# Kernel tuning notes

Measured on AMD Instinct MI355X. Metric: run time of the kernel, lower is better.

## Reference

```python
import jax, jax.numpy as jnp
import numpy as np

B, T, D = 4, 4096, 512

def setup_inputs() -> dict:
    key = jax.random.key(0)
    k1, k2, k3 = jax.random.split(key, 3)
    z_hat = jax.random.normal(k1, (B, T, D), dtype=jnp.float32)
    P = jax.random.uniform(k2, (B, T), dtype=jnp.float32)
    lengths = jax.random.randint(k3, (B,), 0, T).astype(jnp.int32)
    return {"z_hat": z_hat, "P": P, "lengths": lengths}

def reference(z_hat, P, lengths):
    # z_hat: [B, T, D], P: [B, T], lengths: [B]
    Bs, Tc, _ = z_hat.shape
    P_clamped = jnp.clip(P, 0.0, 1.0 - 1e-6)
    q = 1.0 - P_clamped
    # inclusive cumulative sum of log q (same as padded-cumsum[:,1:] in torch)
    log_cumprod_q = jnp.cumsum(jnp.log(q), axis=1)                 # [B, T]
    log_P = jnp.log(jnp.clip(P_clamped, 1e-6, None))               # [B, T]
    # log_M[b, t, k] = log P[b, k] + logcum[b, t] - logcum[b, k], causal (k <= t)
    log_M = (log_P[:, None, :]
             + log_cumprod_q[:, :, None]
             - log_cumprod_q[:, None, :])                          # [B, T, T]
    t_idx = jnp.arange(Tc)
    causal = t_idx[:, None] >= t_idx[None, :]                      # k <= t kept
    M = jnp.where(causal[None, :, :], jnp.exp(log_M), 0.0)         # [B, T, T]
    z_bar = jnp.einsum('btk,bkd->btd', M, z_hat)                   # [B, T, D]
    padding_mask = t_idx[None, :] < lengths[:, None]               # [B, T]
    return z_bar * padding_mask[:, :, None].astype(z_bar.dtype)
```

## Files before the change

### kernel.cpp

```cpp
#include <hip/hip_runtime.h>


#define CHUNK 16
#define NCMAX 512

__global__ __launch_bounds__(128) void k_local(
    const float* __restrict__ z, const float* __restrict__ P,
    const int* __restrict__ lengths,
    float* __restrict__ S, float* __restrict__ A,
    float* __restrict__ out, int B, int T, int D4, int NC) {
  const int blk = blockIdx.x;
  const int b = blk / NC, c = blk % NC;
  const int t0 = c * CHUNK;
  const int tid = threadIdx.x;
  const int L = lengths[b];
  const int nt = min(CHUNK, T - t0);
  const float4 zero = make_float4(0.f, 0.f, 0.f, 0.f);
  const size_t rowbase = ((size_t)b * T + t0) * D4;

  if (t0 >= L) {
    float4* o4 = (float4*)out;
    if (tid < D4)
      for (int t = 0; t < nt; ++t) o4[rowbase + (size_t)t * D4 + tid] = zero;
    return;
  }

  __shared__ float p_s[CHUNK], q_s[CHUNK];
  if (tid < CHUNK) {
    int tg = t0 + tid;
    float p = (tg < T) ? P[(size_t)b * T + tg] : 0.0f;
    p = fminf(fmaxf(p, 0.0f), 1.0f - 1e-6f);
    q_s[tid] = 1.0f - p;
    p_s[tid] = fmaxf(p, 1e-6f);
  }
  __syncthreads();

  if (tid < D4) {
    const float4* z4 = (const float4*)z;
    float4 zr[CHUNK];
#pragma unroll
    for (int t = 0; t < CHUNK; ++t)
      if (t < nt) zr[t] = z4[rowbase + (size_t)t * D4 + tid];
    float4 s = zero;
#pragma unroll
    for (int t = 0; t < CHUNK; ++t)
      if (t < nt) {
        float q = q_s[t], pe = p_s[t];
        s.x = fmaf(q, s.x, pe * zr[t].x);
        s.y = fmaf(q, s.y, pe * zr[t].y);
        s.z = fmaf(q, s.z, pe * zr[t].z);
        s.w = fmaf(q, s.w, pe * zr[t].w);
      }
    ((float4*)S)[((size_t)b * NC + c) * D4 + tid] = s;
  }
  if (tid == 0) {
    float r = 1.0f;
    for (int t = 0; t < nt; ++t) r *= q_s[t];
    A[b * NC + c] = r;
  }
}

__global__ __launch_bounds__(128) void k_apply(
    const float* __restrict__ z, const float* __restrict__ P,
    const float* __restrict__ S, const float* __restrict__ A,
    const int* __restrict__ lengths, float* __restrict__ out,
    int B, int T, int D4, int NC) {
  const int blk = blockIdx.x;
  const int b = blk / NC, c = blk % NC;
  const int t0 = c * CHUNK;
  const int tid = threadIdx.x;
  const int L = lengths[b];
  if (t0 >= L) return;
  const int nt = min(CHUNK, T - t0);
  const float4 zero = make_float4(0.f, 0.f, 0.f, 0.f);

  __shared__ float p_s[CHUNK], q_s[CHUNK];
  __shared__ float a_s[256];
  __shared__ float w_s[256];

  if (tid < CHUNK) {
    int tg = t0 + tid;
    float p = (tg < T) ? P[(size_t)b * T + tg] : 0.0f;
    p = fminf(fmaxf(p, 0.0f), 1.0f - 1e-6f);
    q_s[tid] = 1.0f - p;
    p_s[tid] = fmaxf(p, 1e-6f);
  }
  for (int i = tid; i < NC; i += 128) a_s[i] = A[b * NC + i];
  __syncthreads();

  {
    int i0 = tid, i1 = tid + 128;
    w_s[i0] = (i0 < c - 1) ? a_s[i0 + 1] : 1.0f;
    w_s[i1] = (i1 < c - 1) ? a_s[i1 + 1] : 1.0f;
    __syncthreads();
#pragma unroll
    for (int off = 1; off < 256; off <<= 1) {
      float v0 = (i0 + off < 256) ? w_s[i0 + off] : 1.0f;
      float v1 = (i1 + off < 256) ? w_s[i1 + off] : 1.0f;
      __syncthreads();
      w_s[i0] *= v0;
      w_s[i1] *= v1;
      __syncthreads();
    }
  }

  if (tid < D4) {
    const float4* S4 = (const float4*)S + (size_t)b * NC * D4 + tid;
    float4 a0 = zero, a1 = zero, a2 = zero, a3 = zero;
    int cp = 0;
    for (; cp + 4 <= c; cp += 4) {
      float w0 = w_s[cp], w1 = w_s[cp + 1], w2 = w_s[cp + 2], w3 = w_s[cp + 3];
      float4 r0 = S4[(size_t)cp * D4];
      float4 r1 = S4[(size_t)(cp + 1) * D4];
      float4 r2 = S4[(size_t)(cp + 2) * D4];
      float4 r3 = S4[(size_t)(cp + 3) * D4];
      a0.x = fmaf(w0, r0.x, a0.x); a0.y = fmaf(w0, r0.y, a0.y);
      a0.z = fmaf(w0, r0.z, a0.z); a0.w = fmaf(w0, r0.w, a0.w);
      a1.x = fmaf(w1, r1.x, a1.x); a1.y = fmaf(w1, r1.y, a1.y);
      a1.z = fmaf(w1, r1.z, a1.z); a1.w = fmaf(w1, r1.w, a1.w);
      a2.x = fmaf(w2, r2.x, a2.x); a2.y = fmaf(w2, r2.y, a2.y);
      a2.z = fmaf(w2, r2.z, a2.z); a2.w = fmaf(w2, r2.w, a2.w);
      a3.x = fmaf(w3, r3.x, a3.x); a3.y = fmaf(w3, r3.y, a3.y);
      a3.z = fmaf(w3, r3.z, a3.z); a3.w = fmaf(w3, r3.w, a3.w);
    }
    for (; cp < c; ++cp) {
      float w = w_s[cp];
      float4 r = S4[(size_t)cp * D4];
      a0.x = fmaf(w, r.x, a0.x); a0.y = fmaf(w, r.y, a0.y);
      a0.z = fmaf(w, r.z, a0.z); a0.w = fmaf(w, r.w, a0.w);
    }
    float4 s;
    s.x = (a0.x + a1.x) + (a2.x + a3.x);
    s.y = (a0.y + a1.y) + (a2.y + a3.y);
    s.z = (a0.z + a1.z) + (a2.z + a3.z);
    s.w = (a0.w + a1.w) + (a2.w + a3.w);

    const size_t rowbase = ((size_t)b * T + t0) * D4;
    const float4* z4 = (const float4*)z;
    float4* o4 = (float4*)out;
#pragma unroll
    for (int t = 0; t < CHUNK; ++t)
      if (t < nt) {
        float4 zv = z4[rowbase + (size_t)t * D4 + tid];
        float q = q_s[t], pe = p_s[t];
        s.x = fmaf(q, s.x, pe * zv.x);
        s.y = fmaf(q, s.y, pe * zv.y);
        s.z = fmaf(q, s.z, pe * zv.z);
        s.w = fmaf(q, s.w, pe * zv.w);
        float4 o = ((t0 + t) < L) ? s : zero;
        o4[rowbase + (size_t)t * D4 + tid] = o;
      }
  }
}


__global__ __launch_bounds__(128) void f_local(
    const float* __restrict__ z, const float* __restrict__ P,
    const int* __restrict__ lengths,
    float* __restrict__ S, float* __restrict__ A,
    int B, int T, int D, int NC) {
  int blk = blockIdx.x;
  int b = blk / NC, c = blk % NC;
  int t0 = c * CHUNK;
  int tid = threadIdx.x;
  int D4 = D >> 2;
  float4* S4 = (float4*)(S + ((size_t)b * NC + c) * D);
  int L = lengths[b];
  if (t0 >= L) {
    float4 zero = make_float4(0.f, 0.f, 0.f, 0.f);
    for (int d4 = tid; d4 < D4; d4 += blockDim.x) S4[d4] = zero;
    if (tid == 0) A[b * NC + c] = 1.0f;
    return;
  }
  __shared__ float p_s[CHUNK], q_s[CHUNK];
  if (tid < CHUNK) {
    int tg = t0 + tid;
    float p = (tg < T) ? P[(size_t)b * T + tg] : 0.0f;
    p = fminf(fmaxf(p, 0.0f), 1.0f - 1e-6f);
    q_s[tid] = 1.0f - p;
    p_s[tid] = fmaxf(p, 1e-6f);
  }
  __syncthreads();
  int nt = min(CHUNK, T - t0);
  const float4* z4 = (const float4*)(z + ((size_t)b * T + t0) * D);
  for (int d4 = tid; d4 < D4; d4 += blockDim.x) {
    float4 s = make_float4(0.f, 0.f, 0.f, 0.f);
#pragma unroll
    for (int t = 0; t < CHUNK; ++t) {
      if (t < nt) {
        float4 zv = z4[(size_t)t * D4 + d4];
        float q = q_s[t], pe = p_s[t];
        s.x = fmaf(q, s.x, pe * zv.x);
        s.y = fmaf(q, s.y, pe * zv.y);
        s.z = fmaf(q, s.z, pe * zv.z);
        s.w = fmaf(q, s.w, pe * zv.w);
      }
    }
    S4[d4] = s;
  }
  if (tid == 0) {
    float r = 1.0f;
    for (int t = 0; t < nt; ++t) r *= q_s[t];
    A[b * NC + c] = r;
  }
}

__global__ void f_carry(
    const float* __restrict__ S, const float* __restrict__ A,
    float* __restrict__ Carry, int D4, int NC) {
  int b = blockIdx.x / D4;
  int d4 = blockIdx.x % D4;
  int c = threadIdx.x;
  __shared__ float sh_a[NCMAX];
  __shared__ float4 sh_v[NCMAX];
  float a = A[b * NC + c];
  const float4* S4 = (const float4*)S;
  float4 sv = S4[((size_t)b * NC + c) * D4 + d4];
  sh_a[c] = a;
  sh_v[c] = sv;
  __syncthreads();
  for (int off = 1; off < NC; off <<= 1) {
    float ap = 1.0f;
    float4 vp = make_float4(0.f, 0.f, 0.f, 0.f);
    bool has = (c >= off);
    if (has) { ap = sh_a[c - off]; vp = sh_v[c - off]; }
    __syncthreads();
    if (has) {
      sv.x = fmaf(a, vp.x, sv.x);
      sv.y = fmaf(a, vp.y, sv.y);
      sv.z = fmaf(a, vp.z, sv.z);
      sv.w = fmaf(a, vp.w, sv.w);
      a *= ap;
      sh_a[c] = a;
      sh_v[c] = sv;
    }
    __syncthreads();
  }
  float4 car = make_float4(0.f, 0.f, 0.f, 0.f);
  if (c > 0) car = sh_v[c - 1];
  float4* C4 = (float4*)Carry;
  C4[((size_t)b * NC + c) * D4 + d4] = car;
}

__global__ __launch_bounds__(128) void f_apply(
    const float* __restrict__ z, const float* __restrict__ P,
    const float* __restrict__ Carry, const int* __restrict__ lengths,
    float* __restrict__ out,
    int B, int T, int D, int NC) {
  int blk = blockIdx.x;
  int b = blk / NC, c = blk % NC;
  int t0 = c * CHUNK;
  int tid = threadIdx.x;
  int D4 = D >> 2;
  int nt = min(CHUNK, T - t0);
  float4* o4 = (float4*)(out + ((size_t)b * T + t0) * D);
  int L = lengths[b];
  if (t0 >= L) {
    float4 zero = make_float4(0.f, 0.f, 0.f, 0.f);
    for (int t = 0; t < nt; ++t)
      for (int d4 = tid; d4 < D4; d4 += blockDim.x)
        o4[(size_t)t * D4 + d4] = zero;
    return;
  }
  __shared__ float p_s[CHUNK], q_s[CHUNK];
  if (tid < CHUNK) {
    int tg = t0 + tid;
    float p = (tg < T) ? P[(size_t)b * T + tg] : 0.0f;
    p = fminf(fmaxf(p, 0.0f), 1.0f - 1e-6f);
    q_s[tid] = 1.0f - p;
    p_s[tid] = fmaxf(p, 1e-6f);
  }
  __syncthreads();
  const float4* z4 = (const float4*)(z + ((size_t)b * T + t0) * D);
  const float4* C4 = (const float4*)(Carry + ((size_t)b * NC + c) * D);
  for (int d4 = tid; d4 < D4; d4 += blockDim.x) {
    float4 s = C4[d4];
#pragma unroll
    for (int t = 0; t < CHUNK; ++t) {
      if (t < nt) {
        float4 zv = z4[(size_t)t * D4 + d4];
        float q = q_s[t], pe = p_s[t];
        s.x = fmaf(q, s.x, pe * zv.x);
        s.y = fmaf(q, s.y, pe * zv.y);
        s.z = fmaf(q, s.z, pe * zv.z);
        s.w = fmaf(q, s.w, pe * zv.w);
        float4 o = ((t0 + t) < L) ? s : make_float4(0.f, 0.f, 0.f, 0.f);
        o4[(size_t)t * D4 + d4] = o;
      }
    }
  }
}

extern "C" void kernel_launch(void* const* d_in, const int* in_sizes, int n_in,
                              void* d_out, int out_size, void* d_ws, size_t ws_size,
                              hipStream_t stream) {
  const float* z = (const float*)d_in[0];
  const float* P = (const float*)d_in[1];
  const int* lengths = (const int*)d_in[2];
  float* out = (float*)d_out;

  int B = in_sizes[2];
  int T = in_sizes[1] / B;
  int D = in_sizes[0] / in_sizes[1];
  int NC = (T + CHUNK - 1) / CHUNK;
  int D4 = D >> 2;

  float* S = (float*)d_ws;
  float* A = S + (size_t)B * NC * D;
  float* Carry = A + (((size_t)B * NC + 3) & ~(size_t)3);

  if ((D & 3) == 0 && D4 >= 1 && D4 <= 128 && NC >= 1 && NC <= 256) {
    dim3 grid(B * NC), block(128);
    k_local<<<grid, block, 0, stream>>>(z, P, lengths, S, A, out, B, T, D4, NC);
    k_apply<<<grid, block, 0, stream>>>(z, P, S, A, lengths, out, B, T, D4, NC);
    return;
  }

  f_local<<<dim3(B * NC), dim3(128), 0, stream>>>(z, P, lengths, S, A, B, T, D, NC);
  f_carry<<<dim3(B * D4), dim3(NC), 0, stream>>>(S, A, Carry, D4, NC);
  f_apply<<<dim3(B * NC), dim3(128), 0, stream>>>(z, P, Carry, lengths, out, B, T, D, NC);
}
```

Baseline: 105.2 us.

## Replace two-pass chunked scan with single-pass decoupled look-back scan kernel

Adds a single kernel that computes each chunk's local aggregate, publishes it with a flag, then looks back over predecessor chunks (up to four at a time via wave shuffles) to get an inclusive prefix, and writes the output in the same pass. This drops the second read of z and the per-block recomputation of weights over all previous chunk aggregates that the two-kernel path needed. It also uses nontemporal loads and stores and stops publishing once the chunk passes the sequence length. The cost is spin-waiting on atomics, which assumes earlier blocks are scheduled first and make progress, plus an extra memset launch to clear the flags.

```diff
diff --git a/kernel.cpp b/kernel.cpp
--- a/kernel.cpp
+++ b/kernel.cpp
@@ -2,7 +2,161 @@
 
 
 #define CHUNK 16
-#define NCMAX 512
+
+typedef float f4 __attribute__((ext_vector_type(4)));
+
+__global__ __launch_bounds__(128, 2) void k_scan(
+    const float* __restrict__ z, const float* __restrict__ P,
+    const int* __restrict__ lengths,
+    int* __restrict__ state, float* __restrict__ Apub,
+    float* __restrict__ Sagg, float* __restrict__ Pfx,
+    float* __restrict__ out, int B, int T, int NC) {
+  const int blk = blockIdx.x;
+  const int b = blk / NC, c = blk % NC;
+  const int t0 = c * CHUNK;
+  const int tid = threadIdx.x;
+  const int L = lengths[b];
+  const int nt = min(CHUNK, T - t0);
+  const f4 zero = {0.f, 0.f, 0.f, 0.f};
+  f4* o4 = (f4*)out;
+  const size_t rowbase = ((size_t)b * T + t0) * 128;
+
+  if (t0 >= L) {
+    for (int t = 0; t < nt; ++t)
+      __builtin_nontemporal_store(zero, &o4[rowbase + (size_t)t * 128 + tid]);
+    return;
+  }
+
+  const int nlive = min(nt, L - t0);
+
+  __shared__ float p_s[CHUNK], q_s[CHUNK];
+  if (tid < CHUNK) {
+    float p = (tid < nlive) ? P[(size_t)b * T + t0 + tid] : 0.0f;
+    p = fminf(fmaxf(p, 0.0f), 1.0f - 1e-6f);
+    q_s[tid] = 1.0f - p;
+    p_s[tid] = fmaxf(p, 1e-6f);
+  }
+  __syncthreads();
+
+  const f4* z4 = (const f4*)z;
+  f4 zr[CHUNK];
+#pragma unroll
+  for (int t = 0; t < CHUNK; ++t)
+    if (t < nlive)
+      zr[t] = __builtin_nontemporal_load(&z4[rowbase + (size_t)t * 128 + tid]);
+  f4 s = zero;
+  float a = 1.0f;
+#pragma unroll
+  for (int t = 0; t < CHUNK; ++t)
+    if (t < nlive) {
+      float q = q_s[t], pe = p_s[t];
+      s.x = fmaf(q, s.x, pe * zr[t].x);
+      s.y = fmaf(q, s.y, pe * zr[t].y);
+      s.z = fmaf(q, s.z, pe * zr[t].z);
+      s.w = fmaf(q, s.w, pe * zr[t].w);
+      a *= q;
+    }
+
+  const int idx = b * NC + c;
+  const bool next_live = (t0 + CHUNK < L) && (c + 1 < NC);
+  f4* Sg4 = (f4*)Sagg;
+  f4* Pf4 = (f4*)Pfx;
+
+  if (c > 0 && next_live) {
+    Sg4[(size_t)idx * 128 + tid] = s;
+    if (tid == 0) Apub[idx] = a;
+    __syncthreads();
+    if (tid == 0) {
+      __threadfence();
+      __hip_atomic_store(&state[idx], 1, __ATOMIC_RELEASE, __HIP_MEMORY_SCOPE_AGENT);
+    }
+  }
+
+  f4 carry = zero;
+  if (c > 0) {
+    const int base = b * NC;
+    const int lane = tid & 63;
+    const f4* Sg4c = (const f4*)Sagg;
+    const f4* Pf4c = (const f4*)Pfx;
+    float W = 1.0f;
+    int cp = c - 1;
+    for (;;) {
+      int nb = (cp >= 3) ? 4 : (cp + 1);
+      int off = (lane < nb) ? lane : 0;
+      int stv = __hip_atomic_load(&state[base + cp - off], __ATOMIC_ACQUIRE,
+                                  __HIP_MEMORY_SCOPE_AGENT);
+      int s0 = __shfl(stv, 0);
+      if (s0 == 0) continue;
+      int st1 = (nb > 1) ? __shfl(stv, 1) : 0;
+      int st2 = (nb > 2) ? __shfl(stv, 2) : 0;
+      int st3 = (nb > 3) ? __shfl(stv, 3) : 0;
+      int k = 1;
+      if (st1 != 0) { k = 2; if (st2 != 0) { k = 3; if (st3 != 0) k = 4; } }
+      int m = -1;
+      if (s0 == 2) m = 0;
+      else if (k > 1 && st1 == 2) m = 1;
+      else if (k > 2 && st2 == 2) m = 2;
+      else if (k > 3 && st3 == 2) m = 3;
+      int stop = (m >= 0) ? m : (k - 1);
+      float av = Apub[base + cp - off];
+      float aa[4];
+      aa[0] = __shfl(av, 0); aa[1] = __shfl(av, 1);
+      aa[2] = __shfl(av, 2); aa[3] = __shfl(av, 3);
+      f4 rr[4];
+#pragma unroll
+      for (int i = 0; i < 4; ++i) {
+        int ii = (i <= stop) ? i : stop;
+        size_t ro = (size_t)(base + cp - ii) * 128 + tid;
+        rr[i] = (ii == m) ? Pf4c[ro] : Sg4c[ro];
+      }
+      bool fin = false;
+#pragma unroll
+      for (int i = 0; i < 4; ++i) {
+        if (i <= stop && !fin) {
+          carry.x = fmaf(W, rr[i].x, carry.x);
+          carry.y = fmaf(W, rr[i].y, carry.y);
+          carry.z = fmaf(W, rr[i].z, carry.z);
+          carry.w = fmaf(W, rr[i].w, carry.w);
+          if (i == m) fin = true;
+          else W *= aa[i];
+        }
+      }
+      if (fin) break;
+      cp -= k;
+      if (cp < 0) break;
+    }
+  }
+
+  if (next_live) {
+    f4 f;
+    f.x = fmaf(a, carry.x, s.x);
+    f.y = fmaf(a, carry.y, s.y);
+    f.z = fmaf(a, carry.z, s.z);
+    f.w = fmaf(a, carry.w, s.w);
+    Pf4[(size_t)idx * 128 + tid] = f;
+    __syncthreads();
+    if (tid == 0) {
+      __threadfence();
+      __hip_atomic_store(&state[idx], 2, __ATOMIC_RELEASE, __HIP_MEMORY_SCOPE_AGENT);
+    }
+  }
+
+  f4 sc = carry;
+#pragma unroll
+  for (int t = 0; t < CHUNK; ++t) {
+    if (t < nlive) {
+      float q = q_s[t], pe = p_s[t];
+      sc.x = fmaf(q, sc.x, pe * zr[t].x);
+      sc.y = fmaf(q, sc.y, pe * zr[t].y);
+      sc.z = fmaf(q, sc.z, pe * zr[t].z);
+      sc.w = fmaf(q, sc.w, pe * zr[t].w);
+      __builtin_nontemporal_store(sc, &o4[rowbase + (size_t)t * 128 + tid]);
+    } else if (t < nt) {
+      __builtin_nontemporal_store(zero, &o4[rowbase + (size_t)t * 128 + tid]);
+    }
+  }
+}
+
 
 __global__ __launch_bounds__(128) void k_local(
     const float* __restrict__ z, const float* __restrict__ P,
@@ -24,7 +178,6 @@
       for (int t = 0; t < nt; ++t) o4[rowbase + (size_t)t * D4 + tid] = zero;
     return;
   }
-
   __shared__ float p_s[CHUNK], q_s[CHUNK];
   if (tid < CHUNK) {
     int tg = t0 + tid;
@@ -34,22 +187,18 @@
     p_s[tid] = fmaxf(p, 1e-6f);
   }
   __syncthreads();
-
   if (tid < D4) {
     const float4* z4 = (const float4*)z;
-    float4 zr[CHUNK];
-#pragma unroll
-    for (int t = 0; t < CHUNK; ++t)
-      if (t < nt) zr[t] = z4[rowbase + (size_t)t * D4 + tid];
     float4 s = zero;
 #pragma unroll
     for (int t = 0; t < CHUNK; ++t)
       if (t < nt) {
+        float4 zv = z4[rowbase + (size_t)t * D4 + tid];
         float q = q_s[t], pe = p_s[t];
-        s.x = fmaf(q, s.x, pe * zr[t].x);
-        s.y = fmaf(q, s.y, pe * zr[t].y);
-        s.z = fmaf(q, s.z, pe * zr[t].z);
-        s.w = fmaf(q, s.w, pe * zr[t].w);
+        s.x = fmaf(q, s.x, pe * zv.x);
+        s.y = fmaf(q, s.y, pe * zv.y);
+        s.z = fmaf(q, s.z, pe * zv.z);
+        s.w = fmaf(q, s.w, pe * zv.w);
       }
     ((float4*)S)[((size_t)b * NC + c) * D4 + tid] = s;
   }
@@ -85,9 +234,8 @@
     q_s[tid] = 1.0f - p;
     p_s[tid] = fmaxf(p, 1e-6f);
   }
-  for (int i = tid; i < NC; i += 128) a_s[i] = A[b * NC + i];
+  for (int i = tid; i < NC && i < 256; i += 128) a_s[i] = A[b * NC + i];
   __syncthreads();
-
   {
     int i0 = tid, i1 = tid + 128;
     w_s[i0] = (i0 < c - 1) ? a_s[i0 + 1] : 1.0f;
@@ -103,7 +251,6 @@
       __syncthreads();
     }
   }
-
   if (tid < D4) {
     const float4* S4 = (const float4*)S + (size_t)b * NC * D4 + tid;
     float4 a0 = zero, a1 = zero, a2 = zero, a3 = zero;
@@ -134,7 +281,6 @@
     s.y = (a0.y + a1.y) + (a2.y + a3.y);
     s.z = (a0.z + a1.z) + (a2.z + a3.z);
     s.w = (a0.w + a1.w) + (a2.w + a3.w);
-
     const size_t rowbase = ((size_t)b * T + t0) * D4;
     const float4* z4 = (const float4*)z;
     float4* o4 = (float4*)out;
@@ -153,144 +299,6 @@
   }
 }
 
-
-__global__ __launch_bounds__(128) void f_local(
-    const float* __restrict__ z, const float* __restrict__ P,
-    const int* __restrict__ lengths,
-    float* __restrict__ S, float* __restrict__ A,
-    int B, int T, int D, int NC) {
-  int blk = blockIdx.x;
-  int b = blk / NC, c = blk % NC;
-  int t0 = c * CHUNK;
-  int tid = threadIdx.x;
-  int D4 = D >> 2;
-  float4* S4 = (float4*)(S + ((size_t)b * NC + c) * D);
-  int L = lengths[b];
-  if (t0 >= L) {
-    float4 zero = make_float4(0.f, 0.f, 0.f, 0.f);
-    for (int d4 = tid; d4 < D4; d4 += blockDim.x) S4[d4] = zero;
-    if (tid == 0) A[b * NC + c] = 1.0f;
-    return;
-  }
-  __shared__ float p_s[CHUNK], q_s[CHUNK];
-  if (tid < CHUNK) {
-    int tg = t0 + tid;
-    float p = (tg < T) ? P[(size_t)b * T + tg] : 0.0f;
-    p = fminf(fmaxf(p, 0.0f), 1.0f - 1e-6f);
-    q_s[tid] = 1.0f - p;
-    p_s[tid] = fmaxf(p, 1e-6f);
-  }
-  __syncthreads();
-  int nt = min(CHUNK, T - t0);
-  const float4* z4 = (const float4*)(z + ((size_t)b * T + t0) * D);
-  for (int d4 = tid; d4 < D4; d4 += blockDim.x) {
-    float4 s = make_float4(0.f, 0.f, 0.f, 0.f);
-#pragma unroll
-    for (int t = 0; t < CHUNK; ++t) {
-      if (t < nt) {
-        float4 zv = z4[(size_t)t * D4 + d4];
-        float q = q_s[t], pe = p_s[t];
-        s.x = fmaf(q, s.x, pe * zv.x);
-        s.y = fmaf(q, s.y, pe * zv.y);
-        s.z = fmaf(q, s.z, pe * zv.z);
-        s.w = fmaf(q, s.w, pe * zv.w);
-      }
-    }
-    S4[d4] = s;
-  }
-  if (tid == 0) {
-    float r = 1.0f;
-    for (int t = 0; t < nt; ++t) r *= q_s[t];
-    A[b * NC + c] = r;
-  }
-}
-
-__global__ void f_carry(
-    const float* __restrict__ S, const float* __restrict__ A,
-    float* __restrict__ Carry, int D4, int NC) {
-  int b = blockIdx.x / D4;
-  int d4 = blockIdx.x % D4;
-  int c = threadIdx.x;
-  __shared__ float sh_a[NCMAX];
-  __shared__ float4 sh_v[NCMAX];
-  float a = A[b * NC + c];
-  const float4* S4 = (const float4*)S;
-  float4 sv = S4[((size_t)b * NC + c) * D4 + d4];
-  sh_a[c] = a;
-  sh_v[c] = sv;
-  __syncthreads();
-  for (int off = 1; off < NC; off <<= 1) {
-    float ap = 1.0f;
-    float4 vp = make_float4(0.f, 0.f, 0.f, 0.f);
-    bool has = (c >= off);
-    if (has) { ap = sh_a[c - off]; vp = sh_v[c - off]; }
-    __syncthreads();
-    if (has) {
-      sv.x = fmaf(a, vp.x, sv.x);
-      sv.y = fmaf(a, vp.y, sv.y);
-      sv.z = fmaf(a, vp.z, sv.z);
-      sv.w = fmaf(a, vp.w, sv.w);
-      a *= ap;
-      sh_a[c] = a;
-      sh_v[c] = sv;
-    }
-    __syncthreads();
-  }
-  float4 car = make_float4(0.f, 0.f, 0.f, 0.f);
-  if (c > 0) car = sh_v[c - 1];
-  float4* C4 = (float4*)Carry;
-  C4[((size_t)b * NC + c) * D4 + d4] = car;
-}
-
-__global__ __launch_bounds__(128) void f_apply(
-    const float* __restrict__ z, const float* __restrict__ P,
-    const float* __restrict__ Carry, const int* __restrict__ lengths,
-    float* __restrict__ out,
-    int B, int T, int D, int NC) {
-  int blk = blockIdx.x;
-  int b = blk / NC, c = blk % NC;
-  int t0 = c * CHUNK;
-  int tid = threadIdx.x;
-  int D4 = D >> 2;
-  int nt = min(CHUNK, T - t0);
-  float4* o4 = (float4*)(out + ((size_t)b * T + t0) * D);
-  int L = lengths[b];
-  if (t0 >= L) {
-    float4 zero = make_float4(0.f, 0.f, 0.f, 0.f);
-    for (int t = 0; t < nt; ++t)
-      for (int d4 = tid; d4 < D4; d4 += blockDim.x)
-        o4[(size_t)t * D4 + d4] = zero;
-    return;
-  }
-  __shared__ float p_s[CHUNK], q_s[CHUNK];
-  if (tid < CHUNK) {
-    int tg = t0 + tid;
-    float p = (tg < T) ? P[(size_t)b * T + tg] : 0.0f;
-    p = fminf(fmaxf(p, 0.0f), 1.0f - 1e-6f);
-    q_s[tid] = 1.0f - p;
-    p_s[tid] = fmaxf(p, 1e-6f);
-  }
-  __syncthreads();
-  const float4* z4 = (const float4*)(z + ((size_t)b * T + t0) * D);
-  const float4* C4 = (const float4*)(Carry + ((size_t)b * NC + c) * D);
-  for (int d4 = tid; d4 < D4; d4 += blockDim.x) {
-    float4 s = C4[d4];
-#pragma unroll
-    for (int t = 0; t < CHUNK; ++t) {
-      if (t < nt) {
-        float4 zv = z4[(size_t)t * D4 + d4];
-        float q = q_s[t], pe = p_s[t];
-        s.x = fmaf(q, s.x, pe * zv.x);
-        s.y = fmaf(q, s.y, pe * zv.y);
-        s.z = fmaf(q, s.z, pe * zv.z);
-        s.w = fmaf(q, s.w, pe * zv.w);
-        float4 o = ((t0 + t) < L) ? s : make_float4(0.f, 0.f, 0.f, 0.f);
-        o4[(size_t)t * D4 + d4] = o;
-      }
-    }
-  }
-}
-
 extern "C" void kernel_launch(void* const* d_in, const int* in_sizes, int n_in,
                               void* d_out, int out_size, void* d_ws, size_t ws_size,
                               hipStream_t stream) {
@@ -304,19 +312,25 @@
   int D = in_sizes[0] / in_sizes[1];
   int NC = (T + CHUNK - 1) / CHUNK;
   int D4 = D >> 2;
+  size_t nidx = (size_t)B * NC;
+  size_t nidx4 = (nidx + 3) & ~(size_t)3;
+
+  int* state = (int*)d_ws;
+  float* Apub = (float*)d_ws + nidx4;
+  float* Sagg = Apub + nidx4;
+  float* Pfx = Sagg + nidx * D;
+  size_t need = (nidx4 * 2 + nidx * (size_t)D * 2) * sizeof(float);
+
+  if (D4 == 128 && nidx >= 1 && nidx <= 2048 && ws_size >= need) {
+    (void)hipMemsetAsync(state, 0, nidx * sizeof(int), stream);
+    k_scan<<<dim3((int)nidx), dim3(128), 0, stream>>>(
+        z, P, lengths, state, Apub, Sagg, Pfx, out, B, T, NC);
+    return;
+  }
 
   float* S = (float*)d_ws;
-  float* A = S + (size_t)B * NC * D;
-  float* Carry = A + (((size_t)B * NC + 3) & ~(size_t)3);
-
-  if ((D & 3) == 0 && D4 >= 1 && D4 <= 128 && NC >= 1 && NC <= 256) {
-    dim3 grid(B * NC), block(128);
-    k_local<<<grid, block, 0, stream>>>(z, P, lengths, S, A, out, B, T, D4, NC);
-    k_apply<<<grid, block, 0, stream>>>(z, P, S, A, lengths, out, B, T, D4, NC);
-    return;
-  }
-
-  f_local<<<dim3(B * NC), dim3(128), 0, stream>>>(z, P, lengths, S, A, B, T, D, NC);
-  f_carry<<<dim3(B * D4), dim3(NC), 0, stream>>>(S, A, Carry, D4, NC);
-  f_apply<<<dim3(B * NC), dim3(128), 0, stream>>>(z, P, Carry, lengths, out, B, T, D, NC);
+  float* A = S + nidx * D;
+  dim3 grid((int)nidx), block(128);
+  k_local<<<grid, block, 0, stream>>>(z, P, lengths, S, A, out, B, T, D4, NC);
+  k_apply<<<grid, block, 0, stream>>>(z, P, S, A, lengths, out, B, T, D4, NC);
 }
```

Measured after the change: 250.0 us. 2.38x slower.

## Use 64-row chunks with 4 row-groups per block and warp-shuffle carry scan

Applied to the files above, without the earlier changes.

Replaces the 16-row chunked scan with 64-row chunks handled by 512-thread blocks split into four 16-row groups that combine partial states through shared memory. Fewer chunks shrink the per-batch carry buffer and let the chunk-weight prefix product run as a single 64-lane shuffle scan instead of a barrier-heavy shared-memory scan. The apply kernel prefetches z rows before the carry sum, splits that sum across groups, and writes output with nontemporal stores. The cost is more registers per thread, fewer blocks in the grid, and the local pass now skips S/A for chunks the apply pass does not need.

```diff
diff --git a/kernel.cpp b/kernel.cpp
--- a/kernel.cpp
+++ b/kernel.cpp
@@ -1,20 +1,215 @@
 #include <hip/hip_runtime.h>
 
 
-#define CHUNK 16
-#define NCMAX 512
-
-__global__ __launch_bounds__(128) void k_local(
+#define CHUNK 64
+#define GR 16
+#define NG 4
+#define NCMAX 64
+
+#define FB_CHUNK 16
+#define FB_NCMAX 256
+
+typedef float f4 __attribute__((ext_vector_type(4)));
+
+__global__ __launch_bounds__(512) void kl64(
+    const float* __restrict__ z, const float* __restrict__ P,
+    const int* __restrict__ lengths,
+    float* __restrict__ S, float* __restrict__ A,
+    float* __restrict__ out, int B, int T, int NC) {
+  const int blk = blockIdx.x;
+  const int b = blk / NC, c = blk % NC;
+  const int t0 = c * CHUNK;
+  const int tid = threadIdx.x;
+  const int col = tid & 127, g = tid >> 7;
+  const int L = lengths[b];
+  const int nt = min(CHUNK, T - t0);
+  const f4 zero = {0.f, 0.f, 0.f, 0.f};
+  f4* o4 = (f4*)out;
+  const size_t rowbase = ((size_t)b * T + t0) * 128;
+
+  if (t0 >= L) {
+    for (int r = g; r < nt; r += NG)
+      __builtin_nontemporal_store(zero, &o4[rowbase + (size_t)r * 128 + col]);
+    return;
+  }
+
+  __shared__ float p_s[CHUNK], q_s[CHUNK];
+  __shared__ float ga_s[NG];
+  __shared__ f4 gs_s[NG][128];
+
+  if (tid < CHUNK) {
+    int tg = t0 + tid;
+    float p = (tg < T) ? P[(size_t)b * T + tg] : 0.0f;
+    p = fminf(fmaxf(p, 0.0f), 1.0f - 1e-6f);
+    q_s[tid] = 1.0f - p;
+    p_s[tid] = fmaxf(p, 1e-6f);
+  }
+  __syncthreads();
+
+  const int r0 = g * GR;
+  const int ng = min(GR, nt - r0);
+  const f4* z4 = (const f4*)z;
+  f4 zr[GR];
+#pragma unroll
+  for (int j = 0; j < GR; ++j)
+    if (j < ng) zr[j] = z4[rowbase + (size_t)(r0 + j) * 128 + col];
+  f4 s = zero;
+  float a = 1.0f;
+#pragma unroll
+  for (int j = 0; j < GR; ++j)
+    if (j < ng) {
+      float q = q_s[r0 + j], pe = p_s[r0 + j];
+      s.x = fmaf(q, s.x, pe * zr[j].x);
+      s.y = fmaf(q, s.y, pe * zr[j].y);
+      s.z = fmaf(q, s.z, pe * zr[j].z);
+      s.w = fmaf(q, s.w, pe * zr[j].w);
+      a *= q;
+    }
+  gs_s[g][col] = s;
+  if (col == 0) ga_s[g] = a;
+  __syncthreads();
+
+  if ((t0 + CHUNK < L) && (c + 1 < NC)) {
+    if (g == NG - 1) {
+      f4 x = gs_s[0][col];
+#pragma unroll
+      for (int j = 1; j < NG; ++j) {
+        float aj = ga_s[j];
+        f4 sj = gs_s[j][col];
+        x.x = fmaf(aj, x.x, sj.x);
+        x.y = fmaf(aj, x.y, sj.y);
+        x.z = fmaf(aj, x.z, sj.z);
+        x.w = fmaf(aj, x.w, sj.w);
+      }
+      ((f4*)S)[((size_t)b * NC + c) * 128 + col] = x;
+    }
+    if (tid == 0) A[b * NC + c] = ga_s[0] * ga_s[1] * ga_s[2] * ga_s[3];
+  }
+}
+
+__global__ __launch_bounds__(512) void ka64(
+    const float* __restrict__ z, const float* __restrict__ P,
+    const float* __restrict__ S, const float* __restrict__ A,
+    const int* __restrict__ lengths, float* __restrict__ out,
+    int B, int T, int NC) {
+  const int blk = blockIdx.x;
+  const int b = blk / NC, c = blk % NC;
+  const int t0 = c * CHUNK;
+  const int tid = threadIdx.x;
+  const int col = tid & 127, g = tid >> 7;
+  const int L = lengths[b];
+  if (t0 >= L) return;
+  const int nt = min(CHUNK, T - t0);
+  const f4 zero = {0.f, 0.f, 0.f, 0.f};
+
+  __shared__ float p_s[CHUNK], q_s[CHUNK];
+  __shared__ float sp_s[NCMAX + 1];
+  __shared__ float ga_s[NG];
+  __shared__ f4 gs_s[NG][128];
+  __shared__ f4 part_s[NG][128];
+
+  const int r0 = g * GR;
+  const int ng = min(GR, nt - r0);
+  const f4* z4 = (const f4*)z;
+  const size_t rowbase = ((size_t)b * T + t0) * 128;
+  f4 zr[GR];
+#pragma unroll
+  for (int j = 0; j < GR; ++j)
+    if (j < ng) zr[j] = z4[rowbase + (size_t)(r0 + j) * 128 + col];
+
+  if (tid < CHUNK) {
+    int tg = t0 + tid;
+    float p = (tg < T) ? P[(size_t)b * T + tg] : 0.0f;
+    p = fminf(fmaxf(p, 0.0f), 1.0f - 1e-6f);
+    q_s[tid] = 1.0f - p;
+    p_s[tid] = fmaxf(p, 1e-6f);
+  }
+  if (tid < 64) {
+    const int lane = tid;
+    float y = (lane < c) ? A[b * NC + lane] : 1.0f;
+#pragma unroll
+    for (int off = 1; off < 64; off <<= 1) {
+      float t = __shfl_down(y, off);
+      if (lane + off < 64) y *= t;
+    }
+    sp_s[lane] = y;
+  }
+  __syncthreads();
+
+  f4 acc = zero;
+  const f4* S4 = (const f4*)S;
+  for (int cp = g; cp < c; cp += NG) {
+    float w = sp_s[cp + 1];
+    f4 r = S4[((size_t)b * NC + cp) * 128 + col];
+    acc.x = fmaf(w, r.x, acc.x);
+    acc.y = fmaf(w, r.y, acc.y);
+    acc.z = fmaf(w, r.z, acc.z);
+    acc.w = fmaf(w, r.w, acc.w);
+  }
+  part_s[g][col] = acc;
+
+  f4 s = zero;
+  float a = 1.0f;
+#pragma unroll
+  for (int j = 0; j < GR; ++j)
+    if (j < ng) {
+      float q = q_s[r0 + j], pe = p_s[r0 + j];
+      s.x = fmaf(q, s.x, pe * zr[j].x);
+      s.y = fmaf(q, s.y, pe * zr[j].y);
+      s.z = fmaf(q, s.z, pe * zr[j].z);
+      s.w = fmaf(q, s.w, pe * zr[j].w);
+      a *= q;
+    }
+  gs_s[g][col] = s;
+  if (col == 0) ga_s[g] = a;
+  __syncthreads();
+
+  f4 carry = part_s[0][col];
+  {
+    f4 p1 = part_s[1][col], p2 = part_s[2][col], p3 = part_s[3][col];
+    carry.x = (carry.x + p1.x) + (p2.x + p3.x);
+    carry.y = (carry.y + p1.y) + (p2.y + p3.y);
+    carry.z = (carry.z + p1.z) + (p2.z + p3.z);
+    carry.w = (carry.w + p1.w) + (p2.w + p3.w);
+  }
+#pragma unroll
+  for (int j = 0; j < NG - 1; ++j)
+    if (j < g) {
+      float aj = ga_s[j];
+      f4 sj = gs_s[j][col];
+      carry.x = fmaf(aj, carry.x, sj.x);
+      carry.y = fmaf(aj, carry.y, sj.y);
+      carry.z = fmaf(aj, carry.z, sj.z);
+      carry.w = fmaf(aj, carry.w, sj.w);
+    }
+
+  f4* o4 = (f4*)out;
+  f4 sc = carry;
+#pragma unroll
+  for (int j = 0; j < GR; ++j)
+    if (j < ng) {
+      float q = q_s[r0 + j], pe = p_s[r0 + j];
+      sc.x = fmaf(q, sc.x, pe * zr[j].x);
+      sc.y = fmaf(q, sc.y, pe * zr[j].y);
+      sc.z = fmaf(q, sc.z, pe * zr[j].z);
+      sc.w = fmaf(q, sc.w, pe * zr[j].w);
+      f4 o = ((t0 + r0 + j) < L) ? sc : zero;
+      __builtin_nontemporal_store(o, &o4[rowbase + (size_t)(r0 + j) * 128 + col]);
+    }
+}
+
+
+__global__ __launch_bounds__(128) void k_local_fb(
     const float* __restrict__ z, const float* __restrict__ P,
     const int* __restrict__ lengths,
     float* __restrict__ S, float* __restrict__ A,
     float* __restrict__ out, int B, int T, int D4, int NC) {
   const int blk = blockIdx.x;
   const int b = blk / NC, c = blk % NC;
-  const int t0 = c * CHUNK;
+  const int t0 = c * FB_CHUNK;
   const int tid = threadIdx.x;
   const int L = lengths[b];
-  const int nt = min(CHUNK, T - t0);
+  const int nt = min(FB_CHUNK, T - t0);
   const float4 zero = make_float4(0.f, 0.f, 0.f, 0.f);
   const size_t rowbase = ((size_t)b * T + t0) * D4;
 
@@ -24,9 +219,8 @@
       for (int t = 0; t < nt; ++t) o4[rowbase + (size_t)t * D4 + tid] = zero;
     return;
   }
-
-  __shared__ float p_s[CHUNK], q_s[CHUNK];
-  if (tid < CHUNK) {
+  __shared__ float p_s[FB_CHUNK], q_s[FB_CHUNK];
+  if (tid < FB_CHUNK) {
     int tg = t0 + tid;
     float p = (tg < T) ? P[(size_t)b * T + tg] : 0.0f;
     p = fminf(fmaxf(p, 0.0f), 1.0f - 1e-6f);
@@ -34,22 +228,18 @@
     p_s[tid] = fmaxf(p, 1e-6f);
   }
   __syncthreads();
-
   if (tid < D4) {
     const float4* z4 = (const float4*)z;
-    float4 zr[CHUNK];
-#pragma unroll
-    for (int t = 0; t < CHUNK; ++t)
-      if (t < nt) zr[t] = z4[rowbase + (size_t)t * D4 + tid];
     float4 s = zero;
 #pragma unroll
-    for (int t = 0; t < CHUNK; ++t)
+    for (int t = 0; t < FB_CHUNK; ++t)
       if (t < nt) {
+        float4 zv = z4[rowbase + (size_t)t * D4 + tid];
         float q = q_s[t], pe = p_s[t];
-        s.x = fmaf(q, s.x, pe * zr[t].x);
-        s.y = fmaf(q, s.y, pe * zr[t].y);
-        s.z = fmaf(q, s.z, pe * zr[t].z);
-        s.w = fmaf(q, s.w, pe * zr[t].w);
+        s.x = fmaf(q, s.x, pe * zv.x);
+        s.y = fmaf(q, s.y, pe * zv.y);
+        s.z = fmaf(q, s.z, pe * zv.z);
+        s.w = fmaf(q, s.w, pe * zv.w);
       }
     ((float4*)S)[((size_t)b * NC + c) * D4 + tid] = s;
   }
@@ -60,34 +250,33 @@
   }
 }
 
-__global__ __launch_bounds__(128) void k_apply(
+__global__ __launch_bounds__(128) void k_apply_fb(
     const float* __restrict__ z, const float* __restrict__ P,
     const float* __restrict__ S, const float* __restrict__ A,
     const int* __restrict__ lengths, float* __restrict__ out,
     int B, int T, int D4, int NC) {
   const int blk = blockIdx.x;
   const int b = blk / NC, c = blk % NC;
-  const int t0 = c * CHUNK;
+  const int t0 = c * FB_CHUNK;
   const int tid = threadIdx.x;
   const int L = lengths[b];
   if (t0 >= L) return;
-  const int nt = min(CHUNK, T - t0);
+  const int nt = min(FB_CHUNK, T - t0);
   const float4 zero = make_float4(0.f, 0.f, 0.f, 0.f);
 
-  __shared__ float p_s[CHUNK], q_s[CHUNK];
-  __shared__ float a_s[256];
-  __shared__ float w_s[256];
-
-  if (tid < CHUNK) {
+  __shared__ float p_s[FB_CHUNK], q_s[FB_CHUNK];
+  __shared__ float a_s[FB_NCMAX];
+  __shared__ float w_s[FB_NCMAX];
+
+  if (tid < FB_CHUNK) {
     int tg = t0 + tid;
     float p = (tg < T) ? P[(size_t)b * T + tg] : 0.0f;
     p = fminf(fmaxf(p, 0.0f), 1.0f - 1e-6f);
     q_s[tid] = 1.0f - p;
     p_s[tid] = fmaxf(p, 1e-6f);
   }
-  for (int i = tid; i < NC; i += 128) a_s[i] = A[b * NC + i];
-  __syncthreads();
-
+  for (int i = tid; i < NC && i < FB_NCMAX; i += 128) a_s[i] = A[b * NC + i];
+  __syncthreads();
   {
     int i0 = tid, i1 = tid + 128;
     w_s[i0] = (i0 < c - 1) ? a_s[i0 + 1] : 1.0f;
@@ -103,7 +292,6 @@
       __syncthreads();
     }
   }
-
   if (tid < D4) {
     const float4* S4 = (const float4*)S + (size_t)b * NC * D4 + tid;
     float4 a0 = zero, a1 = zero, a2 = zero, a3 = zero;
@@ -134,12 +322,11 @@
     s.y = (a0.y + a1.y) + (a2.y + a3.y);
     s.z = (a0.z + a1.z) + (a2.z + a3.z);
     s.w = (a0.w + a1.w) + (a2.w + a3.w);
-
     const size_t rowbase = ((size_t)b * T + t0) * D4;
     const float4* z4 = (const float4*)z;
     float4* o4 = (float4*)out;
 #pragma unroll
-    for (int t = 0; t < CHUNK; ++t)
+    for (int t = 0; t < FB_CHUNK; ++t)
       if (t < nt) {
         float4 zv = z4[rowbase + (size_t)t * D4 + tid];
         float q = q_s[t], pe = p_s[t];
@@ -153,144 +340,6 @@
   }
 }
 
-
-__global__ __launch_bounds__(128) void f_local(
-    const float* __restrict__ z, const float* __restrict__ P,
-    const int* __restrict__ lengths,
-    float* __restrict__ S, float* __restrict__ A,
-    int B, int T, int D, int NC) {
-  int blk = blockIdx.x;
-  int b = blk / NC, c = blk % NC;
-  int t0 = c * CHUNK;
-  int tid = threadIdx.x;
-  int D4 = D >> 2;
-  float4* S4 = (float4*)(S + ((size_t)b * NC + c) * D);
-  int L = lengths[b];
-  if (t0 >= L) {
-    float4 zero = make_float4(0.f, 0.f, 0.f, 0.f);
-    for (int d4 = tid; d4 < D4; d4 += blockDim.x) S4[d4] = zero;
-    if (tid == 0) A[b * NC + c] = 1.0f;
-    return;
-  }
-  __shared__ float p_s[CHUNK], q_s[CHUNK];
-  if (tid < CHUNK) {
-    int tg = t0 + tid;
-    float p = (tg < T) ? P[(size_t)b * T + tg] : 0.0f;
-    p = fminf(fmaxf(p, 0.0f), 1.0f - 1e-6f);
-    q_s[tid] = 1.0f - p;
-    p_s[tid] = fmaxf(p, 1e-6f);
-  }
-  __syncthreads();
-  int nt = min(CHUNK, T - t0);
-  const float4* z4 = (const float4*)(z + ((size_t)b * T + t0) * D);
-  for (int d4 = tid; d4 < D4; d4 += blockDim.x) {
-    float4 s = make_float4(0.f, 0.f, 0.f, 0.f);
-#pragma unroll
-    for (int t = 0; t < CHUNK; ++t) {
-      if (t < nt) {
-        float4 zv = z4[(size_t)t * D4 + d4];
-        float q = q_s[t], pe = p_s[t];
-        s.x = fmaf(q, s.x, pe * zv.x);
-        s.y = fmaf(q, s.y, pe * zv.y);
-        s.z = fmaf(q, s.z, pe * zv.z);
-        s.w = fmaf(q, s.w, pe * zv.w);
-      }
-    }
-    S4[d4] = s;
-  }
-  if (tid == 0) {
-    float r = 1.0f;
-    for (int t = 0; t < nt; ++t) r *= q_s[t];
-    A[b * NC + c] = r;
-  }
-}
-
-__global__ void f_carry(
-    const float* __restrict__ S, const float* __restrict__ A,
-    float* __restrict__ Carry, int D4, int NC) {
-  int b = blockIdx.x / D4;
-  int d4 = blockIdx.x % D4;
-  int c = threadIdx.x;
-  __shared__ float sh_a[NCMAX];
-  __shared__ float4 sh_v[NCMAX];
-  float a = A[b * NC + c];
-  const float4* S4 = (const float4*)S;
-  float4 sv = S4[((size_t)b * NC + c) * D4 + d4];
-  sh_a[c] = a;
-  sh_v[c] = sv;
-  __syncthreads();
-  for (int off = 1; off < NC; off <<= 1) {
-    float ap = 1.0f;
-    float4 vp = make_float4(0.f, 0.f, 0.f, 0.f);
-    bool has = (c >= off);
-    if (has) { ap = sh_a[c - off]; vp = sh_v[c - off]; }
-    __syncthreads();
-    if (has) {
-      sv.x = fmaf(a, vp.x, sv.x);
-      sv.y = fmaf(a, vp.y, sv.y);
-      sv.z = fmaf(a, vp.z, sv.z);
-      sv.w = fmaf(a, vp.w, sv.w);
-      a *= ap;
-      sh_a[c] = a;
-      sh_v[c] = sv;
-    }
-    __syncthreads();
-  }
-  float4 car = make_float4(0.f, 0.f, 0.f, 0.f);
-  if (c > 0) car = sh_v[c - 1];
-  float4* C4 = (float4*)Carry;
-  C4[((size_t)b * NC + c) * D4 + d4] = car;
-}
-
-__global__ __launch_bounds__(128) void f_apply(
-    const float* __restrict__ z, const float* __restrict__ P,
-    const float* __restrict__ Carry, const int* __restrict__ lengths,
-    float* __restrict__ out,
-    int B, int T, int D, int NC) {
-  int blk = blockIdx.x;
-  int b = blk / NC, c = blk % NC;
-  int t0 = c * CHUNK;
-  int tid = threadIdx.x;
-  int D4 = D >> 2;
-  int nt = min(CHUNK, T - t0);
-  float4* o4 = (float4*)(out + ((size_t)b * T + t0) * D);
-  int L = lengths[b];
-  if (t0 >= L) {
-    float4 zero = make_float4(0.f, 0.f, 0.f, 0.f);
-    for (int t = 0; t < nt; ++t)
-      for (int d4 = tid; d4 < D4; d4 += blockDim.x)
-        o4[(size_t)t * D4 + d4] = zero;
-    return;
-  }
-  __shared__ float p_s[CHUNK], q_s[CHUNK];
-  if (tid < CHUNK) {
-    int tg = t0 + tid;
-    float p = (tg < T) ? P[(size_t)b * T + tg] : 0.0f;
-    p = fminf(fmaxf(p, 0.0f), 1.0f - 1e-6f);
-    q_s[tid] = 1.0f - p;
-    p_s[tid] = fmaxf(p, 1e-6f);
-  }
-  __syncthreads();
-  const float4* z4 = (const float4*)(z + ((size_t)b * T + t0) * D);
-  const float4* C4 = (const float4*)(Carry + ((size_t)b * NC + c) * D);
-  for (int d4 = tid; d4 < D4; d4 += blockDim.x) {
-    float4 s = C4[d4];
-#pragma unroll
-    for (int t = 0; t < CHUNK; ++t) {
-      if (t < nt) {
-        float4 zv = z4[(size_t)t * D4 + d4];
-        float q = q_s[t], pe = p_s[t];
-        s.x = fmaf(q, s.x, pe * zv.x);
-        s.y = fmaf(q, s.y, pe * zv.y);
-        s.z = fmaf(q, s.z, pe * zv.z);
-        s.w = fmaf(q, s.w, pe * zv.w);
-        float4 o = ((t0 + t) < L) ? s : make_float4(0.f, 0.f, 0.f, 0.f);
-        o4[(size_t)t * D4 + d4] = o;
-      }
-    }
-  }
-}
-
 extern "C" void kernel_launch(void* const* d_in, const int* in_sizes, int n_in,
                               void* d_out, int out_size, void* d_ws, size_t ws_size,
                               hipStream_t stream) {
@@ -302,21 +351,24 @@
   int B = in_sizes[2];
   int T = in_sizes[1] / B;
   int D = in_sizes[0] / in_sizes[1];
-  int NC = (T + CHUNK - 1) / CHUNK;
   int D4 = D >> 2;
 
+  if (D4 == 128) {
+    int NC = (T + CHUNK - 1) / CHUNK;
+    if (NC >= 1 && NC <= NCMAX) {
+      float* S = (float*)d_ws;
+      float* A = S + (size_t)B * NC * D;
+      dim3 grid(B * NC), block(512);
+      kl64<<<grid, block, 0, stream>>>(z, P, lengths, S, A, out, B, T, NC);
+      ka64<<<grid, block, 0, stream>>>(z, P, S, A, lengths, out, B, T, NC);
+      return;
+    }
+  }
+
+  int NC = (T + FB_CHUNK - 1) / FB_CHUNK;
   float* S = (float*)d_ws;
   float* A = S + (size_t)B * NC * D;
-  float* Carry = A + (((size_t)B * NC + 3) & ~(size_t)3);
-
-  if ((D & 3) == 0 && D4 >= 1 && D4 <= 128 && NC >= 1 && NC <= 256) {
-    dim3 grid(B * NC), block(128);
-    k_local<<<grid, block, 0, stream>>>(z, P, lengths, S, A, out, B, T, D4, NC);
-    k_apply<<<grid, block, 0, stream>>>(z, P, S, A, lengths, out, B, T, D4, NC);
-    return;
-  }
-
-  f_local<<<dim3(B * NC), dim3(128), 0, stream>>>(z, P, lengths, S, A, B, T, D, NC);
-  f_carry<<<dim3(B * D4), dim3(NC), 0, stream>>>(S, A, Carry, D4, NC);
-  f_apply<<<dim3(B * NC), dim3(128), 0, stream>>>(z, P, Carry, lengths, out, B, T, D, NC);
-}
+  dim3 grid(B * NC), block(128);
+  k_local_fb<<<grid, block, 0, stream>>>(z, P, lengths, S, A, out, B, T, D4, NC);
+  k_apply_fb<<<grid, block, 0, stream>>>(z, P, S, A, lengths, out, B, T, D4, NC);
+}
```

After: 93.73 us. 10.9% less time.
